# Kernel tuning notes

Measured on AMD Instinct MI355X. Metric: run time of the kernel, lower is better.

The kernel has to match this reference:

```python
import jax, jax.numpy as jnp
import numpy as np

N_EMBED = 1024
HEAD_SIZE = 64


def setup_inputs() -> dict:
    key = jax.random.key(0)
    kx, kq, kk, kv = jax.random.split(key, 4)
    x = jax.random.normal(kx, (8, 2048, N_EMBED), dtype=jnp.float32)
    s = 1.0 / np.sqrt(N_EMBED)
    # nn.Linear weights are [out, in]; store as [in, out] for x @ W
    W_q = jax.random.uniform(kq, (N_EMBED, HEAD_SIZE), jnp.float32, -s, s)
    W_k = jax.random.uniform(kk, (N_EMBED, HEAD_SIZE), jnp.float32, -s, s)
    W_v = jax.random.uniform(kv, (N_EMBED, HEAD_SIZE), jnp.float32, -s, s)
    return {"x": x, "W_q": W_q, "W_k": W_k, "W_v": W_v}


def reference(x, W_q, W_k, W_v):
    b, t, c = x.shape
    q = x @ W_q  # [b, t, h]
    k = x @ W_k
    v = x @ W_v
    scale = k.shape[-1] ** -0.5
    wei = jnp.einsum("bqh,bkh->bqk", q, k) * scale  # [b, t, t]
    causal = jnp.tril(jnp.ones((t, t), dtype=bool))
    wei = jnp.where(causal, wei, -jnp.inf)
    wei = jax.nn.softmax(wei, axis=-1)
    # dropout p=0.0 -> identity
    return jnp.einsum("bqk,bkh->bqh", wei, v)
```

## Files before the change

### kernel.cpp

```cpp
#include <hip/hip_runtime.h>
#include <math.h>

typedef unsigned short u16;
typedef unsigned int u32;
typedef __attribute__((ext_vector_type(4))) float f32x4;
typedef __attribute__((ext_vector_type(8))) short s16x8;
typedef __attribute__((ext_vector_type(4))) unsigned short u16x4;

#define T_ 2048
#define C_ 1024

__device__ __forceinline__ u16 f2b(float f) {
  u32 u = __builtin_bit_cast(u32, f);
  return (u16)((u + 0x8000u) >> 16);
}

__global__ __launch_bounds__(256) void wconv(const float* __restrict__ Wq,
                                             const float* __restrict__ Wk,
                                             const float* __restrict__ Wv,
                                             u16* __restrict__ Wt) {
  int n = blockIdx.x;
  const float* src;
  float scale = 1.0f;
  if (n < 64) { src = Wq; scale = 0.125f; }
  else if (n < 128) { src = Wk; }
  else { src = Wv; }
  int col = n & 63;
  for (int kk = threadIdx.x; kk < C_; kk += 256)
    Wt[(size_t)n * C_ + kk] = f2b(src[(size_t)kk * 64 + col] * scale);
}

__global__ __launch_bounds__(256) void proj(const float* __restrict__ x,
                                            const u16* __restrict__ Wt,
                                            u16* __restrict__ qo,
                                            u16* __restrict__ ko,
                                            u16* __restrict__ vt) {
  __shared__ __align__(16) u16 xs[64 * 72];
  __shared__ __align__(16) u16 ws[192 * 72];
  const int tid = threadIdx.x;
  const int wave = tid >> 6, lane = tid & 63;
  const int quad = lane >> 4, l15 = lane & 15;
  const int m0 = blockIdx.x * 64;

  f32x4 acc[4][3];
#pragma unroll
  for (int m = 0; m < 4; ++m)
#pragma unroll
    for (int j = 0; j < 3; ++j) acc[m][j] = {0.f, 0.f, 0.f, 0.f};

  const int xrow = tid >> 4;
  const int xc4 = (tid & 15) * 4;
  const int wrow = tid >> 3;
  const int wc8 = (tid & 7) * 8;

  float4 xr[4];
  uint4 wr[6];
#pragma unroll
  for (int i = 0; i < 4; ++i)
    xr[i] = *(const float4*)(x + (size_t)(m0 + xrow + i * 16) * C_ + xc4);
#pragma unroll
  for (int i = 0; i < 6; ++i)
    wr[i] = *(const uint4*)(Wt + (size_t)(wrow + i * 32) * C_ + wc8);

  for (int kt = 0; kt < 16; ++kt) {
#pragma unroll
    for (int i = 0; i < 4; ++i) {
      u16x4 pk = {f2b(xr[i].x), f2b(xr[i].y), f2b(xr[i].z), f2b(xr[i].w)};
      *(u16x4*)(&xs[(xrow + i * 16) * 72 + xc4]) = pk;
    }
#pragma unroll
    for (int i = 0; i < 6; ++i)
      *(uint4*)(&ws[(wrow + i * 32) * 72 + wc8]) = wr[i];
    __syncthreads();
    if (kt < 15) {
      const int k1 = (kt + 1) * 64;
#pragma unroll
      for (int i = 0; i < 4; ++i)
        xr[i] = *(const float4*)(x + (size_t)(m0 + xrow + i * 16) * C_ + k1 + xc4);
#pragma unroll
      for (int i = 0; i < 6; ++i)
        wr[i] = *(const uint4*)(Wt + (size_t)(wrow + i * 32) * C_ + k1 + wc8);
    }
#pragma unroll
    for (int ks = 0; ks < 2; ++ks) {
      s16x8 a[4], bfr[3];
#pragma unroll
      for (int m = 0; m < 4; ++m)
        a[m] = *(const s16x8*)(&xs[(l15 + 16 * m) * 72 + ks * 32 + quad * 8]);
#pragma unroll
      for (int j = 0; j < 3; ++j)
        bfr[j] = *(const s16x8*)(&ws[(l15 + 16 * (wave * 3 + j)) * 72 + ks * 32 + quad * 8]);
#pragma unroll
      for (int m = 0; m < 4; ++m)
#pragma unroll
        for (int j = 0; j < 3; ++j)
          acc[m][j] = __builtin_amdgcn_mfma_f32_16x16x32_bf16(a[m], bfr[j], acc[m][j], 0, 0, 0);
    }
    __syncthreads();
  }
#pragma unroll
  for (int m = 0; m < 4; ++m) {
    int rbase = m0 + 16 * m + quad * 4;
#pragma unroll
    for (int j = 0; j < 3; ++j) {
      int ns = wave * 3 + j;
      if (ns < 4) {
        int col = ns * 16 + l15;
#pragma unroll
        for (int i = 0; i < 4; ++i)
          qo[(size_t)(rbase + i) * 64 + col] = f2b(acc[m][j][i]);
      } else if (ns < 8) {
        int col = (ns - 4) * 16 + l15;
#pragma unroll
        for (int i = 0; i < 4; ++i)
          ko[(size_t)(rbase + i) * 64 + col] = f2b(acc[m][j][i]);
      } else {
        int d = (ns - 8) * 16 + l15;
        int bb = m0 >> 11;
        int t0 = (m0 & 2047) + 16 * m + quad * 4;
        u16x4 pk = {f2b(acc[m][j][0]), f2b(acc[m][j][1]),
                    f2b(acc[m][j][2]), f2b(acc[m][j][3])};
        *(u16x4*)(vt + (size_t)bb * (64 * T_) + (size_t)d * T_ + t0) = pk;
      }
    }
  }
}

__global__ __launch_bounds__(256, 1) void attn(const u16* __restrict__ qw,
                                               const u16* __restrict__ kw,
                                               const u16* __restrict__ vt,
                                               float* __restrict__ out) {
  __shared__ __align__(16) u16 Pb[4 * 64 * 72];
  __shared__ float mbuf[4][64];
  __shared__ float lbuf[4][64];
  const int tid = threadIdx.x;
  const int wave = tid >> 6, lane = tid & 63;
  const int quad = lane >> 4, l15 = lane & 15;
  const int qt = blockIdx.x, b = blockIdx.y;

  const u16* qp = qw + ((size_t)b * T_ + qt * 64) * 64;
  const u16* kb = kw + (size_t)b * T_ * 64;
  const u16* vb = vt + (size_t)b * 64 * T_;

  s16x8 qf[4][2];
#pragma unroll
  for (int n = 0; n < 4; ++n)
#pragma unroll
    for (int ks = 0; ks < 2; ++ks)
      qf[n][ks] = *(const s16x8*)(qp + (16 * n + l15) * 64 + ks * 32 + quad * 8);

  f32x4 o[4][4];
  float mr[4], lr[4];
#pragma unroll
  for (int m = 0; m < 4; ++m)
#pragma unroll
    for (int n = 0; n < 4; ++n) o[m][n] = {0.f, 0.f, 0.f, 0.f};
#pragma unroll
  for (int n = 0; n < 4; ++n) { mr[n] = -INFINITY; lr[n] = 0.0f; }

  u16* P = Pb + wave * (64 * 72);

  for (int j = wave; j <= qt; j += 4) {
    const u16* kp = kb + (size_t)j * 64 * 64;
    const u16* vp = vb + j * 64;
    f32x4 s[4][4];
#pragma unroll
    for (int m = 0; m < 4; ++m)
#pragma unroll
      for (int n = 0; n < 4; ++n) s[m][n] = {0.f, 0.f, 0.f, 0.f};
#pragma unroll
    for (int ks = 0; ks < 2; ++ks) {
      s16x8 kf[4];
#pragma unroll
      for (int m = 0; m < 4; ++m)
        kf[m] = *(const s16x8*)(kp + (16 * m + l15) * 64 + ks * 32 + quad * 8);
#pragma unroll
      for (int m = 0; m < 4; ++m)
#pragma unroll
        for (int n = 0; n < 4; ++n)
          s[m][n] = __builtin_amdgcn_mfma_f32_16x16x32_bf16(kf[m], qf[n][ks], s[m][n], 0, 0, 0);
    }
    if (j == qt) {
#pragma unroll
      for (int m = 0; m < 4; ++m)
#pragma unroll
        for (int n = 0; n < 4; ++n)
#pragma unroll
          for (int i = 0; i < 4; ++i)
            if (16 * m + quad * 4 + i > 16 * n + l15) s[m][n][i] = -INFINITY;
    }
    float al[4];
#pragma unroll
    for (int n = 0; n < 4; ++n) {
      float mt = s[0][n][0];
#pragma unroll
      for (int m = 0; m < 4; ++m)
#pragma unroll
        for (int i = 0; i < 4; ++i) mt = fmaxf(mt, s[m][n][i]);
      mt = fmaxf(mt, __shfl_xor(mt, 16));
      mt = fmaxf(mt, __shfl_xor(mt, 32));
      float mn = fmaxf(mr[n], mt);
      al[n] = __expf(mr[n] - mn);
      mr[n] = mn;
      float rs = 0.0f;
#pragma unroll
      for (int m = 0; m < 4; ++m)
#pragma unroll
        for (int i = 0; i < 4; ++i) {
          float p = __expf(s[m][n][i] - mn);
          s[m][n][i] = p;
          rs += p;
        }
      rs += __shfl_xor(rs, 16);
      rs += __shfl_xor(rs, 32);
      lr[n] = lr[n] * al[n] + rs;
    }
#pragma unroll
    for (int n = 0; n < 4; ++n)
#pragma unroll
      for (int m = 0; m < 4; ++m) {
        u16x4 pk = {f2b(s[m][n][0]), f2b(s[m][n][1]), f2b(s[m][n][2]), f2b(s[m][n][3])};
        *(u16x4*)(&P[(16 * n + l15) * 72 + 16 * m + quad * 4]) = pk;
      }
#pragma unroll
    for (int m = 0; m < 4; ++m)
#pragma unroll
      for (int n = 0; n < 4; ++n) o[m][n] *= al[n];
#pragma unroll
    for (int ks = 0; ks < 2; ++ks) {
      s16x8 vf[4], pf[4];
#pragma unroll
      for (int m = 0; m < 4; ++m)
        vf[m] = *(const s16x8*)(vp + (size_t)(16 * m + l15) * T_ + ks * 32 + quad * 8);
#pragma unroll
      for (int n = 0; n < 4; ++n)
        pf[n] = *(const s16x8*)(&P[(16 * n + l15) * 72 + ks * 32 + quad * 8]);
#pragma unroll
      for (int m = 0; m < 4; ++m)
#pragma unroll
        for (int n = 0; n < 4; ++n)
          o[m][n] = __builtin_amdgcn_mfma_f32_16x16x32_bf16(vf[m], pf[n], o[m][n], 0, 0, 0);
    }
  }
  if (quad == 0) {
#pragma unroll
    for (int n = 0; n < 4; ++n) {
      mbuf[wave][16 * n + l15] = mr[n];
      lbuf[wave][16 * n + l15] = lr[n];
    }
  }
  __syncthreads();
#pragma unroll
  for (int m = 0; m < 4; ++m)
#pragma unroll
    for (int n = 0; n < 4; ++n) {
      u16x4 pk = {f2b(o[m][n][0]), f2b(o[m][n][1]), f2b(o[m][n][2]), f2b(o[m][n][3])};
      *(u16x4*)(&Pb[wave * (64 * 72) + (16 * n + l15) * 72 + 16 * m + quad * 4]) = pk;
    }
  __syncthreads();
  const int r = wave * 16 + (lane >> 2);
  const int cg = (lane & 3) * 16;
  float fw[4];
  float mstar = -INFINITY, lsum = 0.0f;
#pragma unroll
  for (int w = 0; w < 4; ++w) mstar = fmaxf(mstar, mbuf[w][r]);
#pragma unroll
  for (int w = 0; w < 4; ++w) {
    fw[w] = __expf(mbuf[w][r] - mstar);
    lsum += fw[w] * lbuf[w][r];
  }
  const float inv = 1.0f / lsum;
  float accv[16];
#pragma unroll
  for (int e = 0; e < 16; ++e) accv[e] = 0.0f;
#pragma unroll
  for (int w = 0; w < 4; ++w) {
#pragma unroll
    for (int h = 0; h < 2; ++h) {
      s16x8 vv = *(const s16x8*)(&Pb[w * (64 * 72) + r * 72 + cg + h * 8]);
#pragma unroll
      for (int e = 0; e < 8; ++e) {
        float f = __builtin_bit_cast(float, ((u32)(u16)vv[e]) << 16);
        accv[h * 8 + e] += fw[w] * f;
      }
    }
  }
  float* op = out + ((size_t)b * T_ + qt * 64 + r) * 64 + cg;
#pragma unroll
  for (int e = 0; e < 16; e += 4) {
    float4 st = {accv[e] * inv, accv[e + 1] * inv, accv[e + 2] * inv, accv[e + 3] * inv};
    *(float4*)(op + e) = st;
  }
}

extern "C" void kernel_launch(void* const* d_in, const int* in_sizes, int n_in,
                              void* d_out, int out_size, void* d_ws, size_t ws_size,
                              hipStream_t stream) {
  const float* x  = (const float*)d_in[0];
  const float* Wq = (const float*)d_in[1];
  const float* Wk = (const float*)d_in[2];
  const float* Wv = (const float*)d_in[3];
  float* out = (float*)d_out;
  char* ws = (char*)d_ws;
  u16* Wt = (u16*)ws;
  u16* q  = (u16*)(ws + 393216);
  u16* k  = (u16*)(ws + 393216 + 2097152);
  u16* vT = (u16*)(ws + 393216 + 2 * 2097152);
  hipLaunchKernelGGL(wconv, dim3(192), dim3(256), 0, stream, Wq, Wk, Wv, Wt);
  hipLaunchKernelGGL(proj, dim3(256), dim3(256), 0, stream, x, Wt, q, k, vT);
  hipLaunchKernelGGL(attn, dim3(32, 8), dim3(256), 0, stream, q, k, vT, out);
}
```

Measured before the change: 160.0 us.

## Rework projection to register-direct MFMA, coalesce weight transpose, use exp2 softmax

```diff
diff --git a/kernel.cpp b/kernel.cpp
--- a/kernel.cpp
+++ b/kernel.cpp
@@ -15,113 +15,113 @@
   return (u16)((u + 0x8000u) >> 16);
 }
 
+__device__ __forceinline__ s16x8 pack8(float4 a, float4 b) {
+  s16x8 r;
+  r[0] = (short)f2b(a.x); r[1] = (short)f2b(a.y);
+  r[2] = (short)f2b(a.z); r[3] = (short)f2b(a.w);
+  r[4] = (short)f2b(b.x); r[5] = (short)f2b(b.y);
+  r[6] = (short)f2b(b.z); r[7] = (short)f2b(b.w);
+  return r;
+}
+
 __global__ __launch_bounds__(256) void wconv(const float* __restrict__ Wq,
                                              const float* __restrict__ Wk,
                                              const float* __restrict__ Wv,
                                              u16* __restrict__ Wt) {
-  int n = blockIdx.x;
-  const float* src;
-  float scale = 1.0f;
-  if (n < 64) { src = Wq; scale = 0.125f; }
-  else if (n < 128) { src = Wk; }
-  else { src = Wv; }
-  int col = n & 63;
-  for (int kk = threadIdx.x; kk < C_; kk += 256)
-    Wt[(size_t)n * C_ + kk] = f2b(src[(size_t)kk * 64 + col] * scale);
-}
-
-__global__ __launch_bounds__(256) void proj(const float* __restrict__ x,
-                                            const u16* __restrict__ Wt,
-                                            u16* __restrict__ qo,
-                                            u16* __restrict__ ko,
-                                            u16* __restrict__ vt) {
-  __shared__ __align__(16) u16 xs[64 * 72];
-  __shared__ __align__(16) u16 ws[192 * 72];
+  __shared__ u16 t[64][68];
+  const int bm = blockIdx.x >> 4;
+  const int kt = blockIdx.x & 15;
+  const float* src = (bm == 0) ? Wq : ((bm == 1) ? Wk : Wv);
+  const float scale = (bm == 0) ? 0.18033688f : 1.0f;
+  const int krow = threadIdx.x >> 2;
+  const int c0 = (threadIdx.x & 3) * 16;
+  const float* sp = src + (size_t)(kt * 64 + krow) * 64 + c0;
+#pragma unroll
+  for (int i = 0; i < 4; ++i) {
+    float4 v = *(const float4*)(sp + i * 4);
+    t[c0 + i * 4 + 0][krow] = f2b(v.x * scale);
+    t[c0 + i * 4 + 1][krow] = f2b(v.y * scale);
+    t[c0 + i * 4 + 2][krow] = f2b(v.z * scale);
+    t[c0 + i * 4 + 3][krow] = f2b(v.w * scale);
+  }
+  __syncthreads();
+  const int n = threadIdx.x >> 2;
+  const int koff = (threadIdx.x & 3) * 16;
+  u16* dst = Wt + (size_t)(bm * 64 + n) * C_ + kt * 64 + koff;
+#pragma unroll
+  for (int i = 0; i < 4; ++i)
+    *(u16x4*)(dst + i * 4) = *(const u16x4*)(&t[n][koff + i * 4]);
+}
+
+__global__ __launch_bounds__(256, 3) void proj(const float* __restrict__ x,
+                                               const u16* __restrict__ Wt,
+                                               u16* __restrict__ qo,
+                                               u16* __restrict__ ko,
+                                               u16* __restrict__ vt) {
   const int tid = threadIdx.x;
   const int wave = tid >> 6, lane = tid & 63;
   const int quad = lane >> 4, l15 = lane & 15;
-  const int m0 = blockIdx.x * 64;
-
-  f32x4 acc[4][3];
-#pragma unroll
-  for (int m = 0; m < 4; ++m)
-#pragma unroll
-    for (int j = 0; j < 3; ++j) acc[m][j] = {0.f, 0.f, 0.f, 0.f};
-
-  const int xrow = tid >> 4;
-  const int xc4 = (tid & 15) * 4;
-  const int wrow = tid >> 3;
-  const int wc8 = (tid & 7) * 8;
-
-  float4 xr[4];
-  uint4 wr[6];
-#pragma unroll
-  for (int i = 0; i < 4; ++i)
-    xr[i] = *(const float4*)(x + (size_t)(m0 + xrow + i * 16) * C_ + xc4);
-#pragma unroll
-  for (int i = 0; i < 6; ++i)
-    wr[i] = *(const uint4*)(Wt + (size_t)(wrow + i * 32) * C_ + wc8);
+  const int m = wave & 1, nh = wave >> 1;
+  const int m0 = blockIdx.x * 32;
+
+  const float* xr = x + (size_t)(m0 + m * 16 + l15) * C_ + quad * 8;
+  const u16* wb = Wt + (size_t)(nh * 96 + l15) * C_ + quad * 8;
+
+  f32x4 acc[6];
+#pragma unroll
+  for (int j = 0; j < 6; ++j) acc[j] = {0.f, 0.f, 0.f, 0.f};
+
+  float4 xn0a = *(const float4*)(xr + 0);
+  float4 xn0b = *(const float4*)(xr + 4);
+  float4 xn1a = *(const float4*)(xr + 32);
+  float4 xn1b = *(const float4*)(xr + 36);
 
   for (int kt = 0; kt < 16; ++kt) {
-#pragma unroll
-    for (int i = 0; i < 4; ++i) {
-      u16x4 pk = {f2b(xr[i].x), f2b(xr[i].y), f2b(xr[i].z), f2b(xr[i].w)};
-      *(u16x4*)(&xs[(xrow + i * 16) * 72 + xc4]) = pk;
-    }
-#pragma unroll
-    for (int i = 0; i < 6; ++i)
-      *(uint4*)(&ws[(wrow + i * 32) * 72 + wc8]) = wr[i];
-    __syncthreads();
+    float4 c0a = xn0a, c0b = xn0b, c1a = xn1a, c1b = xn1b;
     if (kt < 15) {
-      const int k1 = (kt + 1) * 64;
+      const float* p = xr + (kt + 1) * 64;
+      xn0a = *(const float4*)(p + 0);
+      xn0b = *(const float4*)(p + 4);
+      xn1a = *(const float4*)(p + 32);
+      xn1b = *(const float4*)(p + 36);
+    }
+    s16x8 a0 = pack8(c0a, c0b);
+    s16x8 a1 = pack8(c1a, c1b);
+    const u16* wk = wb + kt * 64;
+    s16x8 w0[6], w1[6];
+#pragma unroll
+    for (int j = 0; j < 6; ++j) {
+      w0[j] = *(const s16x8*)(wk + (size_t)j * 16 * C_);
+      w1[j] = *(const s16x8*)(wk + (size_t)j * 16 * C_ + 32);
+    }
+#pragma unroll
+    for (int j = 0; j < 6; ++j)
+      acc[j] = __builtin_amdgcn_mfma_f32_16x16x32_bf16(a0, w0[j], acc[j], 0, 0, 0);
+#pragma unroll
+    for (int j = 0; j < 6; ++j)
+      acc[j] = __builtin_amdgcn_mfma_f32_16x16x32_bf16(a1, w1[j], acc[j], 0, 0, 0);
+  }
+
+  const int r0 = m0 + m * 16 + quad * 4;
+#pragma unroll
+  for (int j = 0; j < 6; ++j) {
+    const int ns = nh * 6 + j;
+    if (ns < 4) {
+      const int col = ns * 16 + l15;
 #pragma unroll
       for (int i = 0; i < 4; ++i)
-        xr[i] = *(const float4*)(x + (size_t)(m0 + xrow + i * 16) * C_ + k1 + xc4);
-#pragma unroll
-      for (int i = 0; i < 6; ++i)
-        wr[i] = *(const uint4*)(Wt + (size_t)(wrow + i * 32) * C_ + k1 + wc8);
-    }
-#pragma unroll
-    for (int ks = 0; ks < 2; ++ks) {
-      s16x8 a[4], bfr[3];
-#pragma unroll
-      for (int m = 0; m < 4; ++m)
-        a[m] = *(const s16x8*)(&xs[(l15 + 16 * m) * 72 + ks * 32 + quad * 8]);
-#pragma unroll
-      for (int j = 0; j < 3; ++j)
-        bfr[j] = *(const s16x8*)(&ws[(l15 + 16 * (wave * 3 + j)) * 72 + ks * 32 + quad * 8]);
-#pragma unroll
-      for (int m = 0; m < 4; ++m)
-#pragma unroll
-        for (int j = 0; j < 3; ++j)
-          acc[m][j] = __builtin_amdgcn_mfma_f32_16x16x32_bf16(a[m], bfr[j], acc[m][j], 0, 0, 0);
-    }
-    __syncthreads();
-  }
-#pragma unroll
-  for (int m = 0; m < 4; ++m) {
-    int rbase = m0 + 16 * m + quad * 4;
-#pragma unroll
-    for (int j = 0; j < 3; ++j) {
-      int ns = wave * 3 + j;
-      if (ns < 4) {
-        int col = ns * 16 + l15;
-#pragma unroll
-        for (int i = 0; i < 4; ++i)
-          qo[(size_t)(rbase + i) * 64 + col] = f2b(acc[m][j][i]);
-      } else if (ns < 8) {
-        int col = (ns - 4) * 16 + l15;
-#pragma unroll
-        for (int i = 0; i < 4; ++i)
-          ko[(size_t)(rbase + i) * 64 + col] = f2b(acc[m][j][i]);
-      } else {
-        int d = (ns - 8) * 16 + l15;
-        int bb = m0 >> 11;
-        int t0 = (m0 & 2047) + 16 * m + quad * 4;
-        u16x4 pk = {f2b(acc[m][j][0]), f2b(acc[m][j][1]),
-                    f2b(acc[m][j][2]), f2b(acc[m][j][3])};
-        *(u16x4*)(vt + (size_t)bb * (64 * T_) + (size_t)d * T_ + t0) = pk;
-      }
+        qo[(size_t)(r0 + i) * 64 + col] = f2b(acc[j][i]);
+    } else if (ns < 8) {
+      const int col = (ns - 4) * 16 + l15;
+#pragma unroll
+      for (int i = 0; i < 4; ++i)
+        ko[(size_t)(r0 + i) * 64 + col] = f2b(acc[j][i]);
+    } else {
+      const int d = (ns - 8) * 16 + l15;
+      const int bb = r0 >> 11;
+      const int t0 = r0 & 2047;
+      u16x4 pk = {f2b(acc[j][0]), f2b(acc[j][1]), f2b(acc[j][2]), f2b(acc[j][3])};
+      *(u16x4*)(vt + (size_t)bb * (64 * T_) + (size_t)d * T_ + t0) = pk;
     }
   }
 }
@@ -200,14 +200,14 @@
       mt = fmaxf(mt, __shfl_xor(mt, 16));
       mt = fmaxf(mt, __shfl_xor(mt, 32));
       float mn = fmaxf(mr[n], mt);
-      al[n] = __expf(mr[n] - mn);
+      al[n] = exp2f(mr[n] - mn);
       mr[n] = mn;
       float rs = 0.0f;
 #pragma unroll
       for (int m = 0; m < 4; ++m)
 #pragma unroll
         for (int i = 0; i < 4; ++i) {
-          float p = __expf(s[m][n][i] - mn);
+          float p = exp2f(s[m][n][i] - mn);
           s[m][n][i] = p;
           rs += p;
         }
@@ -266,7 +266,7 @@
   for (int w = 0; w < 4; ++w) mstar = fmaxf(mstar, mbuf[w][r]);
 #pragma unroll
   for (int w = 0; w < 4; ++w) {
-    fw[w] = __expf(mbuf[w][r] - mstar);
+    fw[w] = exp2f(mbuf[w][r] - mstar);
     lsum += fw[w] * lbuf[w][r];
   }
   const float inv = 1.0f / lsum;
@@ -306,7 +306,7 @@
   u16* q  = (u16*)(ws + 393216);
   u16* k  = (u16*)(ws + 393216 + 2097152);
   u16* vT = (u16*)(ws + 393216 + 2 * 2097152);
-  hipLaunchKernelGGL(wconv, dim3(192), dim3(256), 0, stream, Wq, Wk, Wv, Wt);
-  hipLaunchKernelGGL(proj, dim3(256), dim3(256), 0, stream, x, Wt, q, k, vT);
+  hipLaunchKernelGGL(wconv, dim3(48), dim3(256), 0, stream, Wq, Wk, Wv, Wt);
+  hipLaunchKernelGGL(proj, dim3(512), dim3(256), 0, stream, x, Wt, q, k, vT);
   hipLaunchKernelGGL(attn, dim3(32, 8), dim3(256), 0, stream, q, k, vT, out);
 }
```

New measurement: 180.9 us. 1.13x slower.
